# Performance work log

Measured on AMD Instinct MI355X. Metric: run time of the kernel, lower is better.

The kernel has to match this reference:

```python
import jax, jax.numpy as jnp
import numpy as np

EPSILON = 0.001
CAP = 2000.0
H, W, C, B = 224, 224, 1024, 256


def setup_inputs() -> dict:
    key = jax.random.key(0)
    k1, k2, k3, k4 = jax.random.split(key, 4)
    x = jax.random.normal(k1, (B, H, W), dtype=jnp.float32)
    positions = 0.5 + 0.3 * jax.random.normal(k2, (1, 1, C, 2), dtype=jnp.float32)
    sigmas = 0.02 * jax.random.normal(k3, (1, 1, C), dtype=jnp.float32)
    curve_weights = 0.2 * jax.random.normal(k4, (1, 1, C), dtype=jnp.float32)
    y_axis = jnp.linspace(0.0, 1.0, H + 1)[:-1]
    x_axis = jnp.linspace(0.0, 1.0, W + 1)[:-1]
    ys, xs = jnp.meshgrid(y_axis, x_axis, indexing='ij')
    return {"x": x, "positions": positions, "sigmas": sigmas,
            "curve_weights": curve_weights, "xs": xs.astype(jnp.float32),
            "ys": ys.astype(jnp.float32)}


def calc_curves(positions, sigmas, curve_weights, xs, ys):
    # sigmas/curve_weights: (1,1,C); xs/ys: (H,W)
    two_sig2 = 2.0 * sigmas ** 2 + EPSILON            # (1,1,C)
    factor = 1.0 / (2.0 * jnp.pi * sigmas ** 2 + EPSILON)
    grid = (xs[:, :, None] - positions[..., 1]) ** 2 + \
           (ys[:, :, None] - positions[..., 0]) ** 2   # (H,W,C)
    curves = factor * jnp.exp(-grid / two_sig2) * curve_weights
    return jnp.clip(curves, -CAP, CAP)                 # (H,W,C)


def reference(x, positions, sigmas, curve_weights, xs, ys):
    x = x.reshape(-1, H, W)
    curves = calc_curves(positions, sigmas, curve_weights, xs, ys)
    num_pixels = float(H * W)
    # sum over H,W of curves[None] * x[...,None]  ==  GEMM contraction
    out = jnp.einsum('bhw,hwc->bc', x, curves) / num_pixels
    return out
```

## Files before the change

kernel.cpp:

```cpp
#include <hip/hip_runtime.h>
#include <hip/hip_bf16.h>
#include <stdint.h>

#define HH 224
#define WW 224
#define CC 1024
#define BB 256
#define KK (HH*WW)
#define EPSILON_F 0.001f
#define LOG2E 1.4426950408889634f
#define INVN (1.0f/50176.0f)
#define CLAMP_V (2000.0f/50176.0f)

#define KCHUNKS 32
#define ROWS_PER_CHUNK 7
#define STEPS 49

#define LDS_STRIDE 36

typedef __bf16 bf16x8 __attribute__((ext_vector_type(8)));
typedef float  f32x4  __attribute__((ext_vector_type(4)));

__global__ __launch_bounds__(256)
void cvt_bf16_kernel(const float* __restrict__ x, __hip_bfloat16* __restrict__ xb, int n8) {
    int i = blockIdx.x * 256 + threadIdx.x;
    if (i >= n8) return;
    const float4* p = (const float4*)(x + (size_t)i * 8);
    float4 a = p[0], b = p[1];
    union { __hip_bfloat16 h[8]; uint4 u; } o;
    o.h[0] = (__hip_bfloat16)a.x; o.h[1] = (__hip_bfloat16)a.y;
    o.h[2] = (__hip_bfloat16)a.z; o.h[3] = (__hip_bfloat16)a.w;
    o.h[4] = (__hip_bfloat16)b.x; o.h[5] = (__hip_bfloat16)b.y;
    o.h[6] = (__hip_bfloat16)b.z; o.h[7] = (__hip_bfloat16)b.w;
    *(uint4*)(xb + (size_t)i * 8) = o.u;
}

__global__ __launch_bounds__(256)
void reduce_kernel(const float* __restrict__ part, float* __restrict__ out) {
    int i = blockIdx.x * 256 + threadIdx.x;
    const f32x4* p = (const f32x4*)part + i;
    f32x4 s = {0.f, 0.f, 0.f, 0.f};
#pragma unroll
    for (int z = 0; z < KCHUNKS; ++z)
        s += p[(size_t)z * (BB * CC / 4)];
    ((f32x4*)out)[i] = s;
}

template <bool BF16A, bool PARTIAL>
__global__ __launch_bounds__(256)
void blob_gemm_kernel(const void* __restrict__ xin,
                      const float* __restrict__ pos,
                      const float* __restrict__ sig,
                      const float* __restrict__ cwt,
                      const float* __restrict__ xs,
                      const float* __restrict__ ys,
                      float* __restrict__ dst) {
    __shared__ __bf16 As[2][256 * LDS_STRIDE];
    __shared__ __bf16 Bs[2][64 * LDS_STRIDE];
    __shared__ float  xrow[WW];
    __shared__ float  ycol[ROWS_PER_CHUNK];

    const int tid  = threadIdx.x;
    const int wave = tid >> 6;
    const int lane = tid & 63;

    const int n  = blockIdx.x;
    const int j  = n >> 3;
    const int z  = (n & 7) * 4 + (j >> 4);
    const int c0 = (j & 15) * 64;
    const int k0 = z * (ROWS_PER_CHUNK * WW);

    if (tid < WW) xrow[tid] = xs[tid];
    if (tid >= WW && tid < WW + ROWS_PER_CHUNK)
        ycol[tid - WW] = ys[(z * ROWS_PER_CHUNK + (tid - WW)) * WW];

    const int q   = tid & 3;
    const int cr0 = tid >> 2;
    const int c   = c0 + cr0;
    float A2, S2, P0, P1;
    {
        float s  = sig[c];
        float w  = cwt[c];
        float s2 = s * s;
        A2 = w / (6.283185307179586f * s2 + EPSILON_F) * INVN;
        S2 = LOG2E / (2.0f * s2 + EPSILON_F);
        P0 = pos[2 * c];
        P1 = pos[2 * c + 1];
    }
    const bool doClamp = __any(fabsf(A2) > CLAMP_V) != 0;

    const __hip_bfloat16* agb[4];
    const float* agf[4];
#pragma unroll
    for (int jj = 0; jj < 4; ++jj) {
        size_t off = (size_t)(cr0 + 64 * jj) * KK + k0 + q * 8;
        agb[jj] = (const __hip_bfloat16*)xin + off;
        agf[jj] = (const float*)xin + off;
    }
    const int as_w = cr0 * LDS_STRIDE + q * 8;
    const int bs_w = cr0 * LDS_STRIDE + q * 8;

    const int wm = wave * 64;
    const int fl = lane & 15;
    const int fk = (lane >> 4) * 8;
    const int ar_off = (wm + fl) * LDS_STRIDE + fk;
    const int br_off = fl * LDS_STRIDE + fk;

    f32x4 acc[4][4];
#pragma unroll
    for (int i = 0; i < 4; ++i)
#pragma unroll
        for (int jj = 0; jj < 4; ++jj) acc[i][jj] = (f32x4){0.f, 0.f, 0.f, 0.f};

    __syncthreads();

    float ycolr[ROWS_PER_CHUNK];
#pragma unroll
    for (int r = 0; r < ROWS_PER_CHUNK; ++r) ycolr[r] = ycol[r];

    float Ex[8];
    {
        float4 xv0 = *(const float4*)(xrow + q * 8);
        float4 xv1 = *(const float4*)(xrow + q * 8 + 4);
        float xv[8] = {xv0.x, xv0.y, xv0.z, xv0.w, xv1.x, xv1.y, xv1.z, xv1.w};
#pragma unroll
        for (int i = 0; i < 8; ++i) {
            float dx = xv[i] - P1;
            Ex[i] = __builtin_amdgcn_exp2f(-(dx * S2 * dx));
        }
        float dy  = ycolr[0] - P0;
        float eyA = __builtin_amdgcn_exp2f(-(dy * S2 * dy)) * A2;
        float v[8];
#pragma unroll
        for (int i = 0; i < 8; ++i) v[i] = Ex[i] * eyA;
        if (doClamp) {
#pragma unroll
            for (int i = 0; i < 8; ++i) v[i] = fminf(fmaxf(v[i], -CLAMP_V), CLAMP_V);
        }
        union { __bf16 h[8]; uint4 u; } cv;
#pragma unroll
        for (int i = 0; i < 8; ++i) cv.h[i] = (__bf16)v[i];
        *(uint4*)(&Bs[0][bs_w]) = cv.u;
#pragma unroll
        for (int jj = 0; jj < 4; ++jj) {
            union { __bf16 h[8]; uint4 u; } av;
            if (BF16A) {
                av.u = *(const uint4*)(agb[jj]);
            } else {
                float4 f0 = *(const float4*)(agf[jj]);
                float4 f1 = *(const float4*)(agf[jj] + 4);
                av.h[0] = (__bf16)f0.x; av.h[1] = (__bf16)f0.y;
                av.h[2] = (__bf16)f0.z; av.h[3] = (__bf16)f0.w;
                av.h[4] = (__bf16)f1.x; av.h[5] = (__bf16)f1.y;
                av.h[6] = (__bf16)f1.z; av.h[7] = (__bf16)f1.w;
            }
            *(uint4*)(&As[0][as_w + 64 * jj * LDS_STRIDE]) = av.u;
        }
    }
    __syncthreads();

    int nr = 1, nwb = 0;
#pragma unroll 2
    for (int s = 0; s < STEPS; ++s) {
        const int cb = s & 1;

        uint4  pa[4];
        float4 pf0[4], pf1[4];
        if (s < STEPS - 1) {
            const int koff = nr * WW + nwb * 32;
            if (BF16A) {
#pragma unroll
                for (int jj = 0; jj < 4; ++jj) pa[jj] = *(const uint4*)(agb[jj] + koff);
            } else {
#pragma unroll
                for (int jj = 0; jj < 4; ++jj) {
                    pf0[jj] = *(const float4*)(agf[jj] + koff);
                    pf1[jj] = *(const float4*)(agf[jj] + koff + 4);
                }
            }
        }

        bf16x8 fa[4], fb[4];
#pragma unroll
        for (int i = 0; i < 4; ++i) {
            fa[i] = *(const bf16x8*)(&As[cb][ar_off + i * 16 * LDS_STRIDE]);
            fb[i] = *(const bf16x8*)(&Bs[cb][br_off + i * 16 * LDS_STRIDE]);
        }
#pragma unroll
        for (int mi = 0; mi < 4; ++mi)
#pragma unroll
            for (int ni = 0; ni < 4; ++ni)
                acc[mi][ni] = __builtin_amdgcn_mfma_f32_16x16x32_bf16(
                    fa[mi], fb[ni], acc[mi][ni], 0, 0, 0);

        if (s < STEPS - 1) {
            if (nr == 0) {
                float4 xv0 = *(const float4*)(xrow + nwb * 32 + q * 8);
                float4 xv1 = *(const float4*)(xrow + nwb * 32 + q * 8 + 4);
                float xv[8] = {xv0.x, xv0.y, xv0.z, xv0.w, xv1.x, xv1.y, xv1.z, xv1.w};
#pragma unroll
                for (int i = 0; i < 8; ++i) {
                    float dx = xv[i] - P1;
                    Ex[i] = __builtin_amdgcn_exp2f(-(dx * S2 * dx));
                }
            }
            float dy  = ycolr[nr] - P0;
            float eyA = __builtin_amdgcn_exp2f(-(dy * S2 * dy)) * A2;
            float v[8];
#pragma unroll
            for (int i = 0; i < 8; ++i) v[i] = Ex[i] * eyA;
            if (doClamp) {
#pragma unroll
                for (int i = 0; i < 8; ++i) v[i] = fminf(fmaxf(v[i], -CLAMP_V), CLAMP_V);
            }
            union { __bf16 h[8]; uint4 u; } cv;
#pragma unroll
            for (int i = 0; i < 8; ++i) cv.h[i] = (__bf16)v[i];
            *(uint4*)(&Bs[cb ^ 1][bs_w]) = cv.u;
#pragma unroll
            for (int jj = 0; jj < 4; ++jj) {
                union { __bf16 h[8]; uint4 u; } av;
                if (BF16A) {
                    av.u = pa[jj];
                } else {
                    av.h[0] = (__bf16)pf0[jj].x; av.h[1] = (__bf16)pf0[jj].y;
                    av.h[2] = (__bf16)pf0[jj].z; av.h[3] = (__bf16)pf0[jj].w;
                    av.h[4] = (__bf16)pf1[jj].x; av.h[5] = (__bf16)pf1[jj].y;
                    av.h[6] = (__bf16)pf1[jj].z; av.h[7] = (__bf16)pf1[jj].w;
                }
                *(uint4*)(&As[cb ^ 1][as_w + 64 * jj * LDS_STRIDE]) = av.u;
            }
            ++nr;
            if (nr == ROWS_PER_CHUNK) { nr = 0; ++nwb; }
        }
        __syncthreads();
    }

    const int orow = (lane >> 4) * 4;
    float* base = PARTIAL ? (dst + (size_t)z * BB * CC) : dst;
#pragma unroll
    for (int mi = 0; mi < 4; ++mi) {
        int m = wm + mi * 16 + orow;
#pragma unroll
        for (int ni = 0; ni < 4; ++ni) {
            int cc = c0 + ni * 16 + fl;
#pragma unroll
            for (int v = 0; v < 4; ++v) {
                if (PARTIAL)
                    base[(size_t)(m + v) * CC + cc] = acc[mi][ni][v];
                else
                    atomicAdd(base + (size_t)(m + v) * CC + cc, acc[mi][ni][v]);
            }
        }
    }
}

extern "C" void kernel_launch(void* const* d_in, const int* in_sizes, int n_in,
                              void* d_out, int out_size, void* d_ws, size_t ws_size,
                              hipStream_t stream) {
    const float* x   = (const float*)d_in[0];
    const float* pos = (const float*)d_in[1];
    const float* sg  = (const float*)d_in[2];
    const float* cw  = (const float*)d_in[3];
    const float* xs  = (const float*)d_in[4];
    const float* ys  = (const float*)d_in[5];
    float* out = (float*)d_out;

    dim3 grid(16 * KCHUNKS);
    const size_t nx   = (size_t)BB * KK;
    const size_t XB   = nx * sizeof(__hip_bfloat16);
    const size_t PART = (size_t)KCHUNKS * BB * CC * 4;
    const int n8 = (int)(nx / 8);

    if (ws_size >= PART) {
        float* part = (float*)d_ws;
        blob_gemm_kernel<false, true><<<grid, 256, 0, stream>>>(x, pos, sg, cw, xs, ys, part);
        reduce_kernel<<<BB * CC / 4 / 256, 256, 0, stream>>>(part, out);
    } else if (ws_size >= XB) {
        __hip_bfloat16* xb = (__hip_bfloat16*)d_ws;
        hipMemsetAsync(out, 0, (size_t)BB * CC * sizeof(float), stream);
        cvt_bf16_kernel<<<(n8 + 255) / 256, 256, 0, stream>>>(x, xb, n8);
        blob_gemm_kernel<true, false><<<grid, 256, 0, stream>>>(xb, pos, sg, cw, xs, ys, out);
    } else {
        hipMemsetAsync(out, 0, (size_t)BB * CC * sizeof(float), stream);
        blob_gemm_kernel<false, false><<<grid, 256, 0, stream>>>(x, pos, sg, cw, xs, ys, out);
    }
}
```

Before: 150.0 us.

## Load A fragments directly from global into registers, drop A LDS staging

The x operand (A matrix) no longer goes through shared memory. Each lane loads its MFMA fragment straight from global memory into registers, prefetched one step ahead. This removes the LDS writes, the LDS reads and the LDS footprint for A. The launcher also adds a new preferred path that converts x to bf16 first and then runs the partial-sum GEMM, which halves the A bytes read per step but adds an extra conversion pass over x. The direct loads use 16-byte per-lane strided accesses across rows, so global coalescing becomes worse than with the cooperative tile load.

```diff
diff --git a/kernel.cpp b/kernel.cpp
--- a/kernel.cpp
+++ b/kernel.cpp
@@ -55,7 +55,6 @@
                       const float* __restrict__ xs,
                       const float* __restrict__ ys,
                       float* __restrict__ dst) {
-    __shared__ __bf16 As[2][256 * LDS_STRIDE];
     __shared__ __bf16 Bs[2][64 * LDS_STRIDE];
     __shared__ float  xrow[WW];
     __shared__ float  ycol[ROWS_PER_CHUNK];
@@ -89,23 +88,22 @@
     }
     const bool doClamp = __any(fabsf(A2) > CLAMP_V) != 0;
 
-    const __hip_bfloat16* agb[4];
-    const float* agf[4];
-#pragma unroll
-    for (int jj = 0; jj < 4; ++jj) {
-        size_t off = (size_t)(cr0 + 64 * jj) * KK + k0 + q * 8;
-        agb[jj] = (const __hip_bfloat16*)xin + off;
-        agf[jj] = (const float*)xin + off;
-    }
-    const int as_w = cr0 * LDS_STRIDE + q * 8;
     const int bs_w = cr0 * LDS_STRIDE + q * 8;
 
     const int wm = wave * 64;
     const int fl = lane & 15;
     const int fk = (lane >> 4) * 8;
-    const int ar_off = (wm + fl) * LDS_STRIDE + fk;
     const int br_off = fl * LDS_STRIDE + fk;
 
+    const __hip_bfloat16* afb[4];
+    const float* aff[4];
+#pragma unroll
+    for (int mi = 0; mi < 4; ++mi) {
+        size_t off = (size_t)(wm + fl + mi * 16) * KK + k0 + fk;
+        afb[mi] = (const __hip_bfloat16*)xin + off;
+        aff[mi] = (const float*)xin + off;
+    }
+
     f32x4 acc[4][4];
 #pragma unroll
     for (int i = 0; i < 4; ++i)
@@ -118,6 +116,20 @@
 #pragma unroll
     for (int r = 0; r < ROWS_PER_CHUNK; ++r) ycolr[r] = ycol[r];
 
+    bf16x8 fa[4];
+#pragma unroll
+    for (int mi = 0; mi < 4; ++mi) {
+        if (BF16A) {
+            fa[mi] = *(const bf16x8*)(afb[mi]);
+        } else {
+            float4 f0 = *(const float4*)(aff[mi]);
+            float4 f1 = *(const float4*)(aff[mi] + 4);
+            bf16x8 t;
+            t[0] = (__bf16)f0.x; t[1] = (__bf16)f0.y; t[2] = (__bf16)f0.z; t[3] = (__bf16)f0.w;
+            t[4] = (__bf16)f1.x; t[5] = (__bf16)f1.y; t[6] = (__bf16)f1.z; t[7] = (__bf16)f1.w;
+            fa[mi] = t;
+        }
+    }
     float Ex[8];
     {
         float4 xv0 = *(const float4*)(xrow + q * 8);
@@ -141,21 +153,6 @@
 #pragma unroll
         for (int i = 0; i < 8; ++i) cv.h[i] = (__bf16)v[i];
         *(uint4*)(&Bs[0][bs_w]) = cv.u;
-#pragma unroll
-        for (int jj = 0; jj < 4; ++jj) {
-            union { __bf16 h[8]; uint4 u; } av;
-            if (BF16A) {
-                av.u = *(const uint4*)(agb[jj]);
-            } else {
-                float4 f0 = *(const float4*)(agf[jj]);
-                float4 f1 = *(const float4*)(agf[jj] + 4);
-                av.h[0] = (__bf16)f0.x; av.h[1] = (__bf16)f0.y;
-                av.h[2] = (__bf16)f0.z; av.h[3] = (__bf16)f0.w;
-                av.h[4] = (__bf16)f1.x; av.h[5] = (__bf16)f1.y;
-                av.h[6] = (__bf16)f1.z; av.h[7] = (__bf16)f1.w;
-            }
-            *(uint4*)(&As[0][as_w + 64 * jj * LDS_STRIDE]) = av.u;
-        }
     }
     __syncthreads();
 
@@ -170,28 +167,20 @@
             const int koff = nr * WW + nwb * 32;
             if (BF16A) {
 #pragma unroll
-                for (int jj = 0; jj < 4; ++jj) pa[jj] = *(const uint4*)(agb[jj] + koff);
+                for (int mi = 0; mi < 4; ++mi) pa[mi] = *(const uint4*)(afb[mi] + koff);
             } else {
 #pragma unroll
-                for (int jj = 0; jj < 4; ++jj) {
-                    pf0[jj] = *(const float4*)(agf[jj] + koff);
-                    pf1[jj] = *(const float4*)(agf[jj] + koff + 4);
-                }
-            }
-        }
-
-        bf16x8 fa[4], fb[4];
-#pragma unroll
-        for (int i = 0; i < 4; ++i) {
-            fa[i] = *(const bf16x8*)(&As[cb][ar_off + i * 16 * LDS_STRIDE]);
+                for (int mi = 0; mi < 4; ++mi) {
+                    pf0[mi] = *(const float4*)(aff[mi] + koff);
+                    pf1[mi] = *(const float4*)(aff[mi] + koff + 4);
+                }
+            }
+        }
+
+        bf16x8 fb[4];
+#pragma unroll
+        for (int i = 0; i < 4; ++i)
             fb[i] = *(const bf16x8*)(&Bs[cb][br_off + i * 16 * LDS_STRIDE]);
-        }
-#pragma unroll
-        for (int mi = 0; mi < 4; ++mi)
-#pragma unroll
-            for (int ni = 0; ni < 4; ++ni)
-                acc[mi][ni] = __builtin_amdgcn_mfma_f32_16x16x32_bf16(
-                    fa[mi], fb[ni], acc[mi][ni], 0, 0, 0);
 
         if (s < STEPS - 1) {
             if (nr == 0) {
@@ -217,21 +206,35 @@
 #pragma unroll
             for (int i = 0; i < 8; ++i) cv.h[i] = (__bf16)v[i];
             *(uint4*)(&Bs[cb ^ 1][bs_w]) = cv.u;
-#pragma unroll
-            for (int jj = 0; jj < 4; ++jj) {
-                union { __bf16 h[8]; uint4 u; } av;
-                if (BF16A) {
-                    av.u = pa[jj];
-                } else {
-                    av.h[0] = (__bf16)pf0[jj].x; av.h[1] = (__bf16)pf0[jj].y;
-                    av.h[2] = (__bf16)pf0[jj].z; av.h[3] = (__bf16)pf0[jj].w;
-                    av.h[4] = (__bf16)pf1[jj].x; av.h[5] = (__bf16)pf1[jj].y;
-                    av.h[6] = (__bf16)pf1[jj].z; av.h[7] = (__bf16)pf1[jj].w;
-                }
-                *(uint4*)(&As[cb ^ 1][as_w + 64 * jj * LDS_STRIDE]) = av.u;
-            }
             ++nr;
             if (nr == ROWS_PER_CHUNK) { nr = 0; ++nwb; }
+        }
+
+#pragma unroll
+        for (int mi = 0; mi < 4; ++mi)
+#pragma unroll
+            for (int ni = 0; ni < 4; ++ni)
+                acc[mi][ni] = __builtin_amdgcn_mfma_f32_16x16x32_bf16(
+                    fa[mi], fb[ni], acc[mi][ni], 0, 0, 0);
+
+        if (s < STEPS - 1) {
+            if (BF16A) {
+#pragma unroll
+                for (int mi = 0; mi < 4; ++mi) {
+                    union { uint4 u; bf16x8 h; } t; t.u = pa[mi];
+                    fa[mi] = t.h;
+                }
+            } else {
+#pragma unroll
+                for (int mi = 0; mi < 4; ++mi) {
+                    bf16x8 t;
+                    t[0] = (__bf16)pf0[mi].x; t[1] = (__bf16)pf0[mi].y;
+                    t[2] = (__bf16)pf0[mi].z; t[3] = (__bf16)pf0[mi].w;
+                    t[4] = (__bf16)pf1[mi].x; t[5] = (__bf16)pf1[mi].y;
+                    t[6] = (__bf16)pf1[mi].z; t[7] = (__bf16)pf1[mi].w;
+                    fa[mi] = t;
+                }
+            }
         }
         __syncthreads();
     }
@@ -272,7 +275,13 @@
     const size_t PART = (size_t)KCHUNKS * BB * CC * 4;
     const int n8 = (int)(nx / 8);
 
-    if (ws_size >= PART) {
+    if (ws_size >= XB + PART) {
+        __hip_bfloat16* xb = (__hip_bfloat16*)d_ws;
+        float* part = (float*)((char*)d_ws + XB);
+        cvt_bf16_kernel<<<(n8 + 255) / 256, 256, 0, stream>>>(x, xb, n8);
+        blob_gemm_kernel<true, true><<<grid, 256, 0, stream>>>(xb, pos, sg, cw, xs, ys, part);
+        reduce_kernel<<<BB * CC / 4 / 256, 256, 0, stream>>>(part, out);
+    } else if (ws_size >= PART) {
         float* part = (float*)d_ws;
         blob_gemm_kernel<false, true><<<grid, 256, 0, stream>>>(x, pos, sg, cw, xs, ys, part);
         reduce_kernel<<<BB * CC / 4 / 256, 256, 0, stream>>>(part, out);
```

New measurement: 149.6 us. No clear change (-0.3%).
